# Performance work log

Measured on AMD Instinct MI355X. Metric: run time of the kernel, lower is better.

The kernel has to match this reference:

```python
import jax, jax.numpy as jnp
import numpy as np

B, C, W, H = 8, 256, 128, 128
CR = C // 8  # squeeze channels
EPS = 1e-5   # InstanceNorm2d default eps


def _dw_conv(x, w, b, dil):
    # depthwise 3x3 dilated conv, NCHW, kernel [C,1,3,3], 'same' padding = dil
    out = jax.lax.conv_general_dilated(
        x, w, window_strides=(1, 1),
        padding=[(dil, dil), (dil, dil)],
        rhs_dilation=(dil, dil),
        dimension_numbers=("NCHW", "OIHW", "NCHW"),
        feature_group_count=x.shape[1])
    return out + b[None, :, None, None]


def setup_inputs() -> dict:
    key = jax.random.key(0)
    ks = jax.random.split(key, 9)
    s = 0.1
    return {
        "x": jax.random.normal(ks[0], (B, C, W, H), jnp.float32),
        "wq": jax.random.normal(ks[1], (C, 1, 3, 3), jnp.float32) * s,
        "bq": jax.random.normal(ks[2], (C,), jnp.float32) * s,
        "wk": jax.random.normal(ks[3], (C, 1, 3, 3), jnp.float32) * s,
        "bk": jax.random.normal(ks[4], (C,), jnp.float32) * s,
        "w_sq": jax.random.normal(ks[5], (CR, C), jnp.float32) * s,
        "b_sq": jax.random.normal(ks[6], (CR,), jnp.float32) * s,
        "w_ex": jax.random.normal(ks[7], (C, CR), jnp.float32) * s,
        "b_ex": jax.random.normal(ks[8], (C,), jnp.float32) * s,
    }


def reference(x, wq, bq, wk, bk, w_sq, b_sq, w_ex, b_ex):
    b, c, w, h = x.shape
    q = _dw_conv(x, wq, bq, 3)   # [B,C,W,H], dilation 3
    k = _dw_conv(x, wk, bk, 6)   # [B,C,W,H], dilation 6
    # per-channel QK matmul: contracts q's last dim with k's second-to-last (requires W==H)
    attn = jnp.einsum("bcij,bcjk->bcik", q, k)  # [B,C,W,H]
    # softmax over flattened spatial dims per (b, c)
    attn = jax.nn.softmax(attn.reshape(b, c, w * h), axis=-1).reshape(b, c, w, h)
    # channel global average pool of key, broadcast-multiply
    pool = jnp.mean(k, axis=(2, 3), keepdims=True)  # [B,C,1,1]
    y = attn * pool
    # 1x1 squeeze conv C -> C//8
    s = jnp.einsum("bcwh,dc->bdwh", y, w_sq) + b_sq[None, :, None, None]
    # InstanceNorm2d (no affine, biased variance over spatial dims)
    mu = jnp.mean(s, axis=(2, 3), keepdims=True)
    var = jnp.var(s, axis=(2, 3), keepdims=True)
    s = jax.nn.relu((s - mu) * jax.lax.rsqrt(var + EPS))
    # 1x1 expand conv C//8 -> C
    out = jnp.einsum("bdwh,cd->bcwh", s, w_ex) + b_ex[None, :, None, None]
    return out
```

## Files before the change

kernel.cpp:

```cpp
#include <hip/hip_runtime.h>
#include <cstdint>

#define WDIM 128
#define NPX  16384
#define XSTR 132
#define QSTR 136
#define XPAD 16
#define LDS_A_BYTES 69888

typedef __attribute__((ext_vector_type(8))) short short8;
typedef __attribute__((ext_vector_type(4))) float f32x4;

__device__ __forceinline__ float wave_max(float v) {
#pragma unroll
  for (int m = 32; m >= 1; m >>= 1) v = fmaxf(v, __shfl_xor(v, m));
  return v;
}
__device__ __forceinline__ float wave_sum(float v) {
#pragma unroll
  for (int m = 32; m >= 1; m >>= 1) v += __shfl_xor(v, m);
  return v;
}
__device__ __forceinline__ unsigned short f2bf(float f) {
  uint32_t u = __float_as_uint(f);
  return (unsigned short)((u + 0x7fff + ((u >> 16) & 1)) >> 16);
}
__device__ __forceinline__ float bf2f(unsigned short h) {
  return __uint_as_float(((uint32_t)h) << 16);
}
__device__ __forceinline__ float sgpr_f(float v) {
  return __uint_as_float(__builtin_amdgcn_readfirstlane(__float_as_uint(v)));
}

__device__ __forceinline__ void load_win(float* xw, const float* xq, int rr,
                                         int c0h, bool mlo, bool mhi) {
  const float* bp = &xq[rr * XSTR + c0h - 8];
#pragma unroll
  for (int k = 0; k < 8; ++k) *(float4*)&xw[4 * k] = *(const float4*)&bp[4 * k];
  if (mlo) {
#pragma unroll
    for (int j = 0; j < 8; ++j) xw[j] = 0.f;
  }
  if (mhi) {
#pragma unroll
    for (int j = 24; j < 32; ++j) xw[j] = 0.f;
  }
}

template <int OFF>
__device__ __forceinline__ void tap16(float* acc, const float* xw, float w) {
#pragma unroll
  for (int i = 0; i < 16; ++i) acc[i] = fmaf(w, xw[8 + OFF + i], acc[i]);
}

__global__ __launch_bounds__(512, 4)
void kA(const float* __restrict__ x, const float* __restrict__ wq,
        const float* __restrict__ bq, const float* __restrict__ wk,
        const float* __restrict__ bk, unsigned short* __restrict__ y) {
  extern __shared__ char smem[];
  float* xq = (float*)smem + XPAD;
  unsigned short* qb = (unsigned short*)smem;
  unsigned short* kt = (unsigned short*)(smem + 34816);
  float* red = (float*)(smem + 69632);

  const int bc = blockIdx.x;
  const int t = threadIdx.x;
  const float* __restrict__ xp = x + (size_t)bc * NPX;

#pragma unroll
  for (int it = 0; it < 8; ++it) {
    int i = (t + it * 512) * 4;
    int rr = i >> 7, c = i & 127;
    *(float4*)&xq[rr * XSTR + c] = *(const float4*)&xp[i];
  }

  const int ch = bc & 255;
  float q9[9], k9[9];
#pragma unroll
  for (int i = 0; i < 9; ++i) {
    q9[i] = sgpr_f(wq[ch * 9 + i]);
    k9[i] = sgpr_f(wk[ch * 9 + i]);
  }
  const float bqv = sgpr_f(bq[ch]), bkv = sgpr_f(bk[ch]);
  __syncthreads();

  const int r = t >> 2, cb = t & 3;
  float aq[32], ak[32];
#pragma unroll
  for (int i = 0; i < 32; ++i) { aq[i] = bqv; ak[i] = bkv; }

#pragma unroll
  for (int h = 0; h < 2; ++h) {
    const int c0h = cb * 32 + h * 16;
    const bool mlo = (cb == 0) && (h == 0);
    const bool mhi = (cb == 3) && (h == 1);
    float* aqh = aq + h * 16;
    float* akh = ak + h * 16;
    float xw[32];
    if (r >= 6) {
      load_win(xw, xq, r - 6, c0h, mlo, mhi);
      tap16<-6>(akh, xw, k9[0]); tap16<0>(akh, xw, k9[1]); tap16<6>(akh, xw, k9[2]);
    }
    if (r >= 3) {
      load_win(xw, xq, r - 3, c0h, mlo, mhi);
      tap16<-3>(aqh, xw, q9[0]); tap16<0>(aqh, xw, q9[1]); tap16<3>(aqh, xw, q9[2]);
    }
    {
      load_win(xw, xq, r, c0h, mlo, mhi);
      tap16<-3>(aqh, xw, q9[3]); tap16<0>(aqh, xw, q9[4]); tap16<3>(aqh, xw, q9[5]);
      tap16<-6>(akh, xw, k9[3]); tap16<0>(akh, xw, k9[4]); tap16<6>(akh, xw, k9[5]);
    }
    if (r < 125) {
      load_win(xw, xq, r + 3, c0h, mlo, mhi);
      tap16<-3>(aqh, xw, q9[6]); tap16<0>(aqh, xw, q9[7]); tap16<3>(aqh, xw, q9[8]);
    }
    if (r < 122) {
      load_win(xw, xq, r + 6, c0h, mlo, mhi);
      tap16<-6>(akh, xw, k9[6]); tap16<0>(akh, xw, k9[7]); tap16<6>(akh, xw, k9[8]);
    }
  }

  float psum = 0.f;
#pragma unroll
  for (int i = 0; i < 32; ++i) psum += ak[i];

  __syncthreads();

#pragma unroll
  for (int g = 0; g < 4; ++g) {
    short8 pk;
#pragma unroll
    for (int j = 0; j < 8; ++j) pk[j] = (short)f2bf(aq[g * 8 + j]);
    *(short8*)&qb[r * QSTR + cb * 32 + g * 8] = pk;
  }
#pragma unroll
  for (int i = 0; i < 32; ++i) kt[(cb * 32 + i) * QSTR + r] = f2bf(ak[i]);
  __syncthreads();

  const int w = t >> 6, lane = t & 63;
  const int wr = w >> 2, wc = w & 3;
  const int r16 = lane & 15, kg = lane >> 4;
  f32x4 acc[4][2];
#pragma unroll
  for (int mi = 0; mi < 4; ++mi)
#pragma unroll
    for (int ni = 0; ni < 2; ++ni) acc[mi][ni] = (f32x4){0.f, 0.f, 0.f, 0.f};

#pragma unroll
  for (int kk = 0; kk < 4; ++kk) {
    const int kb = kk * 32 + kg * 8;
    short8 a0 = *(const short8*)&qb[(wr * 64 + 0 * 16 + r16) * QSTR + kb];
    short8 a1 = *(const short8*)&qb[(wr * 64 + 1 * 16 + r16) * QSTR + kb];
    short8 a2 = *(const short8*)&qb[(wr * 64 + 2 * 16 + r16) * QSTR + kb];
    short8 a3 = *(const short8*)&qb[(wr * 64 + 3 * 16 + r16) * QSTR + kb];
    short8 b0 = *(const short8*)&kt[(wc * 32 + 0 + r16) * QSTR + kb];
    short8 b1 = *(const short8*)&kt[(wc * 32 + 16 + r16) * QSTR + kb];
    acc[0][0] = __builtin_amdgcn_mfma_f32_16x16x32_bf16(a0, b0, acc[0][0], 0, 0, 0);
    acc[0][1] = __builtin_amdgcn_mfma_f32_16x16x32_bf16(a0, b1, acc[0][1], 0, 0, 0);
    acc[1][0] = __builtin_amdgcn_mfma_f32_16x16x32_bf16(a1, b0, acc[1][0], 0, 0, 0);
    acc[1][1] = __builtin_amdgcn_mfma_f32_16x16x32_bf16(a1, b1, acc[1][1], 0, 0, 0);
    acc[2][0] = __builtin_amdgcn_mfma_f32_16x16x32_bf16(a2, b0, acc[2][0], 0, 0, 0);
    acc[2][1] = __builtin_amdgcn_mfma_f32_16x16x32_bf16(a2, b1, acc[2][1], 0, 0, 0);
    acc[3][0] = __builtin_amdgcn_mfma_f32_16x16x32_bf16(a3, b0, acc[3][0], 0, 0, 0);
    acc[3][1] = __builtin_amdgcn_mfma_f32_16x16x32_bf16(a3, b1, acc[3][1], 0, 0, 0);
  }

  float amax = -3.402823466e38f;
#pragma unroll
  for (int mi = 0; mi < 4; ++mi)
#pragma unroll
    for (int ni = 0; ni < 2; ++ni)
#pragma unroll
      for (int j = 0; j < 4; ++j) amax = fmaxf(amax, acc[mi][ni][j]);
  amax = wave_max(amax);
  if (lane == 0) red[w] = amax;
  __syncthreads();
  float bmax = red[0];
#pragma unroll
  for (int w2 = 1; w2 < 8; ++w2) bmax = fmaxf(bmax, red[w2]);

  float es = 0.f;
#pragma unroll
  for (int mi = 0; mi < 4; ++mi)
#pragma unroll
    for (int ni = 0; ni < 2; ++ni)
#pragma unroll
      for (int j = 0; j < 4; ++j) {
        float e = __expf(acc[mi][ni][j] - bmax);
        acc[mi][ni][j] = e;
        es += e;
      }
  es = wave_sum(es);
  float ps = wave_sum(psum);
  if (lane == 0) { red[8 + w] = es; red[16 + w] = ps; }
  __syncthreads();
  float tsum = 0.f, tpool = 0.f;
#pragma unroll
  for (int w2 = 0; w2 < 8; ++w2) { tsum += red[8 + w2]; tpool += red[16 + w2]; }
  const float scale = (tpool * (1.f / 16384.f)) / tsum;

  unsigned short* __restrict__ yp = y + (size_t)bc * NPX;
#pragma unroll
  for (int mi = 0; mi < 4; ++mi)
#pragma unroll
    for (int ni = 0; ni < 2; ++ni) {
      const int col = wc * 32 + ni * 16 + r16;
#pragma unroll
      for (int j = 0; j < 4; ++j) {
        const int row = wr * 64 + mi * 16 + kg * 4 + j;
        yp[row * WDIM + col] = f2bf(acc[mi][ni][j] * scale);
      }
    }
}

__global__ __launch_bounds__(256, 2)
void kS(const unsigned short* __restrict__ y, const float* __restrict__ w_sq,
        unsigned short* __restrict__ sT, float* __restrict__ partials) {
  __shared__ unsigned short yT[64][264];
  __shared__ float red[256];
  const int t = threadIdx.x;
  const int w = t >> 6, lane = t & 63;
  const int r16 = lane & 15, kg = lane >> 4;
  const int b = blockIdx.x >> 6;
  const int chunk = blockIdx.x & 63;
  const unsigned short* __restrict__ yb = y + (size_t)b * 256 * NPX;

  short8 aw[2][8];
#pragma unroll
  for (int mt = 0; mt < 2; ++mt)
#pragma unroll
    for (int ks = 0; ks < 8; ++ks) {
      const float* p = &w_sq[(mt * 16 + r16) * 256 + ks * 32 + kg * 8];
      float4 f0 = *(const float4*)p;
      float4 f1 = *(const float4*)(p + 4);
      short8 a;
      a[0] = f2bf(f0.x); a[1] = f2bf(f0.y); a[2] = f2bf(f0.z); a[3] = f2bf(f0.w);
      a[4] = f2bf(f1.x); a[5] = f2bf(f1.y); a[6] = f2bf(f1.z); a[7] = f2bf(f1.w);
      aw[mt][ks] = a;
    }

  float ssum[8], ssq[8];
#pragma unroll
  for (int i = 0; i < 8; ++i) { ssum[i] = 0.f; ssq[i] = 0.f; }

  for (int st = 0; st < 4; ++st) {
    const int p0 = chunk * 256 + st * 64;
#pragma unroll
    for (int it = 0; it < 8; ++it) {
      const int tid = it * 4 + w;
      const int cg = tid & 3, pg = tid >> 2;
      const int c = cg * 64 + lane;
      short8 v = *(const short8*)&yb[(size_t)c * NPX + p0 + pg * 8];
#pragma unroll
      for (int j = 0; j < 8; ++j) yT[pg * 8 + j][c] = (unsigned short)v[j];
    }
    __syncthreads();

    f32x4 acc[2][4];
#pragma unroll
    for (int mi = 0; mi < 2; ++mi)
#pragma unroll
      for (int ni = 0; ni < 4; ++ni) acc[mi][ni] = (f32x4){0.f, 0.f, 0.f, 0.f};

#pragma unroll
    for (int ks = 0; ks < 8; ++ks) {
#pragma unroll
      for (int ni = 0; ni < 4; ++ni) {
        short8 bv = *(const short8*)&yT[ni * 16 + r16][ks * 32 + kg * 8];
        acc[0][ni] = __builtin_amdgcn_mfma_f32_16x16x32_bf16(aw[0][ks], bv, acc[0][ni], 0, 0, 0);
        acc[1][ni] = __builtin_amdgcn_mfma_f32_16x16x32_bf16(aw[1][ks], bv, acc[1][ni], 0, 0, 0);
      }
    }

#pragma unroll
    for (int mi = 0; mi < 2; ++mi)
#pragma unroll
      for (int ni = 0; ni < 4; ++ni) {
        const int px = p0 + ni * 16 + r16;
        ushort4 pk;
#pragma unroll
        for (int j = 0; j < 4; ++j) {
          float v = acc[mi][ni][j];
          ssum[mi * 4 + j] += v;
          ssq[mi * 4 + j] += v * v;
          ((unsigned short*)&pk)[j] = f2bf(v);
        }
        *(ushort4*)&sT[((size_t)b * NPX + px) * 32 + mi * 16 + kg * 4] = pk;
      }
    __syncthreads();
  }

#pragma unroll
  for (int i = 0; i < 8; ++i) {
    float sm = ssum[i], sq = ssq[i];
#pragma unroll
    for (int m = 8; m >= 1; m >>= 1) {
      sm += __shfl_xor(sm, m);
      sq += __shfl_xor(sq, m);
    }
    if (r16 == 0) {
      const int d = (i >> 2) * 16 + kg * 4 + (i & 3);
      red[w * 64 + d] = sm;
      red[w * 64 + 32 + d] = sq;
    }
  }
  __syncthreads();
  if (t < 64) {
    float tot = red[t] + red[64 + t] + red[128 + t] + red[192 + t];
    partials[(size_t)blockIdx.x * 64 + t] = tot;
  }
}

__global__ void kR(const float* __restrict__ partials, float* __restrict__ mu_rs) {
  const int b = blockIdx.x, d = threadIdx.x;
  float sm = 0.f, sq = 0.f;
  for (int ch = 0; ch < 64; ++ch) {
    const float* pp = &partials[(size_t)(b * 64 + ch) * 64];
    sm += pp[d];
    sq += pp[32 + d];
  }
  float m = sm * (1.f / 16384.f);
  float v = sq * (1.f / 16384.f) - m * m;
  mu_rs[b * 64 + d] = m;
  mu_rs[b * 64 + 32 + d] = rsqrtf(v + 1e-5f);
}

__global__ __launch_bounds__(256, 3)
void kO(const unsigned short* __restrict__ sT, const float* __restrict__ mu_rs,
        const float* __restrict__ w_ex, const float* __restrict__ b_ex,
        float* __restrict__ out) {
  const int t = threadIdx.x;
  const int w = t >> 6, lane = t & 63;
  const int r16 = lane & 15, kg = lane >> 4;
  const int b = blockIdx.x >> 8;
  const int p0 = (blockIdx.x & 255) * 64;
  const int c0 = w * 64;

  short8 aw[4];
#pragma unroll
  for (int mt = 0; mt < 4; ++mt) {
    const int c = c0 + mt * 16 + r16;
    const float* p = &w_ex[c * 32 + kg * 8];
    float4 f0 = *(const float4*)p;
    float4 f1 = *(const float4*)(p + 4);
    short8 a;
    a[0] = f2bf(f0.x); a[1] = f2bf(f0.y); a[2] = f2bf(f0.z); a[3] = f2bf(f0.w);
    a[4] = f2bf(f1.x); a[5] = f2bf(f1.y); a[6] = f2bf(f1.z); a[7] = f2bf(f1.w);
    aw[mt] = a;
  }

  float m8[8], r8[8];
  {
    const float* mp = &mu_rs[b * 64 + kg * 8];
    const float* rp = &mu_rs[b * 64 + 32 + kg * 8];
#pragma unroll
    for (int q = 0; q < 8; ++q) { m8[q] = mp[q]; r8[q] = rp[q]; }
  }

  f32x4 acc[4][4];
#pragma unroll
  for (int mt = 0; mt < 4; ++mt)
#pragma unroll
    for (int ni = 0; ni < 4; ++ni) acc[mt][ni] = (f32x4){0.f, 0.f, 0.f, 0.f};

#pragma unroll
  for (int ni = 0; ni < 4; ++ni) {
    const int px = p0 + ni * 16 + r16;
    short8 sv = *(const short8*)&sT[((size_t)b * NPX + px) * 32 + kg * 8];
    short8 hb;
#pragma unroll
    for (int q = 0; q < 8; ++q) {
      float f = bf2f((unsigned short)sv[q]);
      float h = fmaxf((f - m8[q]) * r8[q], 0.f);
      hb[q] = f2bf(h);
    }
#pragma unroll
    for (int mt = 0; mt < 4; ++mt)
      acc[mt][ni] = __builtin_amdgcn_mfma_f32_16x16x32_bf16(aw[mt], hb, acc[mt][ni], 0, 0, 0);
  }

  float* __restrict__ ob = out + (size_t)b * 256 * NPX;
#pragma unroll
  for (int mt = 0; mt < 4; ++mt) {
#pragma unroll
    for (int j = 0; j < 4; ++j) {
      const int c = c0 + mt * 16 + kg * 4 + j;
      const float bv = b_ex[c];
#pragma unroll
      for (int ni = 0; ni < 4; ++ni) {
        const int px = p0 + ni * 16 + r16;
        ob[(size_t)c * NPX + px] = acc[mt][ni][j] + bv;
      }
    }
  }
}

extern "C" void kernel_launch(void* const* d_in, const int* in_sizes, int n_in,
                              void* d_out, int out_size, void* d_ws, size_t ws_size,
                              hipStream_t stream) {
  (void)in_sizes; (void)n_in; (void)out_size; (void)ws_size;
  const float* x    = (const float*)d_in[0];
  const float* wq   = (const float*)d_in[1];
  const float* bq   = (const float*)d_in[2];
  const float* wk   = (const float*)d_in[3];
  const float* bk   = (const float*)d_in[4];
  const float* w_sq = (const float*)d_in[5];
  const float* w_ex = (const float*)d_in[7];
  const float* b_ex = (const float*)d_in[8];
  float* out = (float*)d_out;

  unsigned short* sT = (unsigned short*)d_ws;
  float* partials = (float*)((char*)d_ws + (size_t)8 * NPX * 32 * 2);
  float* mu_rs = partials + (size_t)512 * 64;

  unsigned short* ybf = (unsigned short*)d_out;

  hipFuncSetAttribute((const void*)kA, hipFuncAttributeMaxDynamicSharedMemorySize,
                      LDS_A_BYTES);

  kA<<<2048, 512, LDS_A_BYTES, stream>>>(x, wq, bq, wk, bk, ybf);
  kS<<<512, 256, 0, stream>>>(ybf, w_sq, sT, partials);
  kR<<<8, 32, 0, stream>>>(partials, mu_rs);
  kO<<<2048, 256, 0, stream>>>(sT, mu_rs, w_ex, b_ex, out);
}
```

Before: 148.5 us.

## Read conv input rows directly from global memory instead of staging in LDS

The depthwise dilated conv stage now reads its input windows straight from global memory (through cache) rather than first copying the whole 128x128 plane into shared memory. This removes the staging copy and two barriers and shrinks the LDS allocation. Boundary rows are handled by clamping pointers and zeroing tap weights, so no branches are needed. The q and k results are now written to shared memory per half-tile, which lowers register pressure. The trade-off is that each thread makes repeated uncoalesced-ish global/L2 reads of overlapping rows, about five times per element, where before each element was read once into LDS.

```diff
diff --git a/kernel.cpp b/kernel.cpp
--- a/kernel.cpp
+++ b/kernel.cpp
@@ -3,10 +3,8 @@
 
 #define WDIM 128
 #define NPX  16384
-#define XSTR 132
 #define QSTR 136
-#define XPAD 16
-#define LDS_A_BYTES 69888
+#define LDS_A_BYTES 69760
 
 typedef __attribute__((ext_vector_type(8))) short short8;
 typedef __attribute__((ext_vector_type(4))) float f32x4;
@@ -32,18 +30,16 @@
   return __uint_as_float(__builtin_amdgcn_readfirstlane(__float_as_uint(v)));
 }
 
-__device__ __forceinline__ void load_win(float* xw, const float* xq, int rr,
-                                         int c0h, bool mlo, bool mhi) {
-  const float* bp = &xq[rr * XSTR + c0h - 8];
-#pragma unroll
-  for (int k = 0; k < 8; ++k) *(float4*)&xw[4 * k] = *(const float4*)&bp[4 * k];
-  if (mlo) {
-#pragma unroll
-    for (int j = 0; j < 8; ++j) xw[j] = 0.f;
-  }
-  if (mhi) {
-#pragma unroll
-    for (int j = 24; j < 32; ++j) xw[j] = 0.f;
+__device__ __forceinline__ void load_win_g(float* xw, const float* rowp,
+                                           int c0h, bool mlo, bool mhi) {
+  const float* bp = rowp + c0h - 8;
+#pragma unroll
+  for (int k = 0; k < 8; ++k) {
+    if ((k < 2 && mlo) || (k >= 6 && mhi)) {
+      xw[4 * k] = 0.f; xw[4 * k + 1] = 0.f; xw[4 * k + 2] = 0.f; xw[4 * k + 3] = 0.f;
+    } else {
+      *(float4*)&xw[4 * k] = *(const float4*)&bp[4 * k];
+    }
   }
 }
 
@@ -58,7 +54,6 @@
         const float* __restrict__ bq, const float* __restrict__ wk,
         const float* __restrict__ bk, unsigned short* __restrict__ y) {
   extern __shared__ char smem[];
-  float* xq = (float*)smem + XPAD;
   unsigned short* qb = (unsigned short*)smem;
   unsigned short* kt = (unsigned short*)(smem + 34816);
   float* red = (float*)(smem + 69632);
@@ -67,13 +62,6 @@
   const int t = threadIdx.x;
   const float* __restrict__ xp = x + (size_t)bc * NPX;
 
-#pragma unroll
-  for (int it = 0; it < 8; ++it) {
-    int i = (t + it * 512) * 4;
-    int rr = i >> 7, c = i & 127;
-    *(float4*)&xq[rr * XSTR + c] = *(const float4*)&xp[i];
-  }
-
   const int ch = bc & 255;
   float q9[9], k9[9];
 #pragma unroll
@@ -82,59 +70,59 @@
     k9[i] = sgpr_f(wk[ch * 9 + i]);
   }
   const float bqv = sgpr_f(bq[ch]), bkv = sgpr_f(bk[ch]);
-  __syncthreads();
 
   const int r = t >> 2, cb = t & 3;
-  float aq[32], ak[32];
-#pragma unroll
-  for (int i = 0; i < 32; ++i) { aq[i] = bqv; ak[i] = bkv; }
-
+
+  float ktm[3], qtm[3], qbm[3], kbm[3];
+#pragma unroll
+  for (int i = 0; i < 3; ++i) {
+    ktm[i] = (r >= 6)  ? k9[i]     : 0.f;
+    qtm[i] = (r >= 3)  ? q9[i]     : 0.f;
+    qbm[i] = (r < 125) ? q9[6 + i] : 0.f;
+    kbm[i] = (r < 122) ? k9[6 + i] : 0.f;
+  }
+  const float* rm6 = xp + (r >= 6 ? r - 6 : 0) * WDIM;
+  const float* rm3 = xp + (r >= 3 ? r - 3 : 0) * WDIM;
+  const float* r00 = xp + r * WDIM;
+  const float* rp3 = xp + (r < 125 ? r + 3 : 127) * WDIM;
+  const float* rp6 = xp + (r < 122 ? r + 6 : 127) * WDIM;
+
+  float psum = 0.f;
 #pragma unroll
   for (int h = 0; h < 2; ++h) {
     const int c0h = cb * 32 + h * 16;
     const bool mlo = (cb == 0) && (h == 0);
     const bool mhi = (cb == 3) && (h == 1);
-    float* aqh = aq + h * 16;
-    float* akh = ak + h * 16;
+    float aqh[16], akh[16];
+#pragma unroll
+    for (int i = 0; i < 16; ++i) { aqh[i] = bqv; akh[i] = bkv; }
+
     float xw[32];
-    if (r >= 6) {
-      load_win(xw, xq, r - 6, c0h, mlo, mhi);
-      tap16<-6>(akh, xw, k9[0]); tap16<0>(akh, xw, k9[1]); tap16<6>(akh, xw, k9[2]);
-    }
-    if (r >= 3) {
-      load_win(xw, xq, r - 3, c0h, mlo, mhi);
-      tap16<-3>(aqh, xw, q9[0]); tap16<0>(aqh, xw, q9[1]); tap16<3>(aqh, xw, q9[2]);
-    }
-    {
-      load_win(xw, xq, r, c0h, mlo, mhi);
-      tap16<-3>(aqh, xw, q9[3]); tap16<0>(aqh, xw, q9[4]); tap16<3>(aqh, xw, q9[5]);
-      tap16<-6>(akh, xw, k9[3]); tap16<0>(akh, xw, k9[4]); tap16<6>(akh, xw, k9[5]);
-    }
-    if (r < 125) {
-      load_win(xw, xq, r + 3, c0h, mlo, mhi);
-      tap16<-3>(aqh, xw, q9[6]); tap16<0>(aqh, xw, q9[7]); tap16<3>(aqh, xw, q9[8]);
-    }
-    if (r < 122) {
-      load_win(xw, xq, r + 6, c0h, mlo, mhi);
-      tap16<-6>(akh, xw, k9[6]); tap16<0>(akh, xw, k9[7]); tap16<6>(akh, xw, k9[8]);
-    }
-  }
-
-  float psum = 0.f;
-#pragma unroll
-  for (int i = 0; i < 32; ++i) psum += ak[i];
-
-  __syncthreads();
-
-#pragma unroll
-  for (int g = 0; g < 4; ++g) {
-    short8 pk;
-#pragma unroll
-    for (int j = 0; j < 8; ++j) pk[j] = (short)f2bf(aq[g * 8 + j]);
-    *(short8*)&qb[r * QSTR + cb * 32 + g * 8] = pk;
-  }
-#pragma unroll
-  for (int i = 0; i < 32; ++i) kt[(cb * 32 + i) * QSTR + r] = f2bf(ak[i]);
+    load_win_g(xw, rm6, c0h, mlo, mhi);
+    tap16<-6>(akh, xw, ktm[0]); tap16<0>(akh, xw, ktm[1]); tap16<6>(akh, xw, ktm[2]);
+    load_win_g(xw, rm3, c0h, mlo, mhi);
+    tap16<-3>(aqh, xw, qtm[0]); tap16<0>(aqh, xw, qtm[1]); tap16<3>(aqh, xw, qtm[2]);
+    load_win_g(xw, r00, c0h, mlo, mhi);
+    tap16<-3>(aqh, xw, q9[3]); tap16<0>(aqh, xw, q9[4]); tap16<3>(aqh, xw, q9[5]);
+    tap16<-6>(akh, xw, k9[3]); tap16<0>(akh, xw, k9[4]); tap16<6>(akh, xw, k9[5]);
+    load_win_g(xw, rp3, c0h, mlo, mhi);
+    tap16<-3>(aqh, xw, qbm[0]); tap16<0>(aqh, xw, qbm[1]); tap16<3>(aqh, xw, qbm[2]);
+    load_win_g(xw, rp6, c0h, mlo, mhi);
+    tap16<-6>(akh, xw, kbm[0]); tap16<0>(akh, xw, kbm[1]); tap16<6>(akh, xw, kbm[2]);
+
+#pragma unroll
+    for (int g = 0; g < 2; ++g) {
+      short8 pk;
+#pragma unroll
+      for (int j = 0; j < 8; ++j) pk[j] = (short)f2bf(aqh[g * 8 + j]);
+      *(short8*)&qb[r * QSTR + c0h + g * 8] = pk;
+    }
+#pragma unroll
+    for (int i = 0; i < 16; ++i) {
+      kt[(c0h + i) * QSTR + r] = f2bf(akh[i]);
+      psum += akh[i];
+    }
+  }
   __syncthreads();
 
   const int w = t >> 6, lane = t & 63;
```

After: 323.6 us. +118.0%, slower.
